# Kernel tuning notes

Hardware: AMD Instinct MI355X
Metric: run time of the kernel (lower is better)

The kernel has to match this reference:

```python
import jax, jax.numpy as jnp
import numpy as np

C_IMG = 16
GRID = 128
NV = 100000
NE = 1600000
CH = (32, 64, 64)
SCALE = 0.1
STEPS = 1
SLOPE = 0.3  # LeakyReLU default in module


def setup_inputs() -> dict:
    key = jax.random.key(0)
    ks = jax.random.split(key, 20)
    image_features = jax.random.normal(ks[0], (C_IMG, GRID, GRID, GRID), jnp.float32)
    # vertices live in voxel coordinates of the feature grid
    vertices = jax.random.uniform(ks[1], (NV, 3), jnp.float32) * (GRID - 1)
    edge_src = jax.random.randint(ks[2], (NE,), 0, NV, jnp.int32)
    edge_dst = jax.random.randint(ks[3], (NE,), 0, NV, jnp.int32)
    dims = [C_IMG + 3] + list(CH) + [3]  # +3 normalized positions
    inp = {"image_features": image_features, "vertices": vertices,
           "edge_src": edge_src, "edge_dst": edge_dst}
    ki = 4
    for i in range(len(dims) - 1):
        fan_in = dims[i]
        s = 1.0 / np.sqrt(fan_in)
        inp[f"w_self{i}"] = jax.random.normal(ks[ki], (dims[i], dims[i + 1]), jnp.float32) * s
        inp[f"w_nb{i}"] = jax.random.normal(ks[ki + 1], (dims[i], dims[i + 1]), jnp.float32) * s
        inp[f"b{i}"] = jnp.zeros((dims[i + 1],), jnp.float32)
        ki += 2
    return inp


def trilinear_sample(img, verts):
    # img: (C, W, H, D); verts: (V, 3) voxel coords -> (V, C)
    C, W, H, D = img.shape
    hi = jnp.array([W - 1, H - 1, D - 1], verts.dtype)
    p = jnp.clip(verts, 0.0, hi)
    p0 = jnp.floor(p)
    i0 = p0.astype(jnp.int32)
    i1 = jnp.minimum(i0 + 1, hi.astype(jnp.int32))
    w = p - p0
    x0, y0, z0 = i0[:, 0], i0[:, 1], i0[:, 2]
    x1, y1, z1 = i1[:, 0], i1[:, 1], i1[:, 2]
    wx, wy, wz = w[:, 0:1], w[:, 1:2], w[:, 2:3]

    def g(xi, yi, zi):
        return img[:, xi, yi, zi].T  # (V, C)

    c00 = g(x0, y0, z0) * (1 - wz) + g(x0, y0, z1) * wz
    c01 = g(x0, y1, z0) * (1 - wz) + g(x0, y1, z1) * wz
    c10 = g(x1, y0, z0) * (1 - wz) + g(x1, y0, z1) * wz
    c11 = g(x1, y1, z0) * (1 - wz) + g(x1, y1, z1) * wz
    return (c00 * (1 - wy) + c01 * wy) * (1 - wx) + (c10 * (1 - wy) + c11 * wy) * wx


def edge_conv(x, src, dst, inv_deg, w_self, w_nb, b):
    nb = jax.ops.segment_sum(x[src], dst, num_segments=x.shape[0]) * inv_deg
    return x @ w_self + nb @ w_nb + b


def reference(image_features, vertices, edge_src, edge_dst,
              w_self0, w_nb0, b0, w_self1, w_nb1, b1,
              w_self2, w_nb2, b2, w_self3, w_nb3, b3):
    nv = vertices.shape[0]
    deg = jax.ops.segment_sum(jnp.ones((edge_src.shape[0],), jnp.float32), edge_dst,
                              num_segments=nv)
    inv_deg = (1.0 / jnp.maximum(deg, 1.0))[:, None]
    grid_max = jnp.float32(max(image_features.shape[1:]))  # image_shape.max()
    layers = [(w_self0, w_nb0, b0), (w_self1, w_nb1, b1), (w_self2, w_nb2, b2)]
    for _ in range(STEPS):
        feats = trilinear_sample(image_features, vertices)
        feats = jnp.concatenate([vertices / grid_max, feats], axis=-1)
        h = feats
        for (ws, wn, b) in layers:
            h = jax.nn.leaky_relu(edge_conv(h, edge_src, edge_dst, inv_deg, ws, wn, b), SLOPE)
        deformation = edge_conv(h, edge_src, edge_dst, inv_deg, w_self3, w_nb3, b3)
        vertices = vertices + SCALE * deformation
    return vertices
```

## Files before the change

kernel.cpp:

```cpp
#include <hip/hip_runtime.h>

#define C_IMG 16
#define GRIDSZ 128
#define VOL (GRIDSZ * GRIDSZ * GRIDSZ)
#define SLOPE 0.3f
#define SCALE 0.1f
#define EPB 4096
#define CAPB 12288
#define BIN_CAP 16384

using f4_t  = __attribute__((ext_vector_type(4))) float;
using bf8_t = __attribute__((ext_vector_type(8))) short;

__device__ __forceinline__ unsigned int bf16_pack2(float a, float b) {
    unsigned int ua = __float_as_uint(a);
    ua = (ua + 0x7FFFu + ((ua >> 16) & 1u)) >> 16;
    unsigned int ub = __float_as_uint(b);
    ub = (ub + 0x7FFFu + ((ub >> 16) & 1u)) >> 16;
    return ua | (ub << 16);
}
__device__ __forceinline__ unsigned short bf16_1(float a) {
    unsigned int ua = __float_as_uint(a);
    return (unsigned short)((ua + 0x7FFFu + ((ua >> 16) & 1u)) >> 16);
}
__device__ __forceinline__ float bf_lo(unsigned int u) { return __uint_as_float(u << 16); }
__device__ __forceinline__ float bf_hi(unsigned int u) { return __uint_as_float(u & 0xFFFF0000u); }

__global__ __launch_bounds__(256) void k_transpose(const float* __restrict__ img,
                                                   unsigned int* __restrict__ timg) {
    const int t = blockIdx.x * 256 + threadIdx.x;
    const int zp = t & 63;
    const int xy = t >> 6;
    const size_t ibase = (size_t)xy * GRIDSZ + 2 * zp;
    float2 c[16];
    #pragma unroll
    for (int ch = 0; ch < 16; ++ch)
        c[ch] = *(const float2*)(img + (size_t)ch * VOL + ibase);
    uint4 o0a, o0b, o1a, o1b;
    o0a.x = bf16_pack2(c[0].x,  c[1].x);  o0a.y = bf16_pack2(c[2].x,  c[3].x);
    o0a.z = bf16_pack2(c[4].x,  c[5].x);  o0a.w = bf16_pack2(c[6].x,  c[7].x);
    o0b.x = bf16_pack2(c[8].x,  c[9].x);  o0b.y = bf16_pack2(c[10].x, c[11].x);
    o0b.z = bf16_pack2(c[12].x, c[13].x); o0b.w = bf16_pack2(c[14].x, c[15].x);
    o1a.x = bf16_pack2(c[0].y,  c[1].y);  o1a.y = bf16_pack2(c[2].y,  c[3].y);
    o1a.z = bf16_pack2(c[4].y,  c[5].y);  o1a.w = bf16_pack2(c[6].y,  c[7].y);
    o1b.x = bf16_pack2(c[8].y,  c[9].y);  o1b.y = bf16_pack2(c[10].y, c[11].y);
    o1b.z = bf16_pack2(c[12].y, c[13].y); o1b.w = bf16_pack2(c[14].y, c[15].y);
    unsigned int* po = timg + (size_t)(xy * GRIDSZ + 2 * zp) * 8;
    *(uint4*)(po + 0)  = o0a;
    *(uint4*)(po + 4)  = o0b;
    *(uint4*)(po + 8)  = o1a;
    *(uint4*)(po + 12) = o1b;
}

__global__ __launch_bounds__(256) void k_bucket(const int* __restrict__ esrc,
                                                const int* __restrict__ edst,
                                                int* __restrict__ bucketCursor,
                                                unsigned int* __restrict__ pairs,
                                                int* __restrict__ rowStart,
                                                int ne, int nv) {
    __shared__ unsigned int hist[256];
    __shared__ unsigned int pref[256];
    __shared__ unsigned int curs[256];
    __shared__ unsigned int gbase[256];
    __shared__ unsigned int stage_v[EPB];
    __shared__ unsigned char stage_b[EPB];
    const int tid = threadIdx.x;
    const int base = blockIdx.x * EPB;
    const int n = min(EPB, ne - base);
    if (blockIdx.x == 0 && tid == 0) rowStart[nv] = ne;
    hist[tid] = 0;
    __syncthreads();
    for (int i = tid; i < n; i += 256)
        atomicAdd(&hist[((unsigned)edst[base + i]) >> 9], 1u);
    __syncthreads();
    const unsigned int h = hist[tid];
    pref[tid] = h;
    __syncthreads();
    #pragma unroll
    for (int off = 1; off < 256; off <<= 1) {
        unsigned int t = (tid >= off) ? pref[tid - off] : 0;
        __syncthreads();
        pref[tid] += t;
        __syncthreads();
    }
    const unsigned int excl = pref[tid] - h;
    if (h) {
        int pos = atomicAdd(&bucketCursor[tid], (int)h);
        if (pos > CAPB - (int)h) pos = CAPB - (int)h;
        gbase[tid] = (unsigned int)(tid * CAPB + pos);
    } else {
        gbase[tid] = 0u;
    }
    __syncthreads();
    pref[tid] = excl;
    curs[tid] = excl;
    __syncthreads();
    for (int i = tid; i < n; i += 256) {
        unsigned int d = (unsigned)edst[base + i];
        unsigned int s = (unsigned)esrc[base + i];
        unsigned int p = atomicAdd(&curs[d >> 9], 1u);
        stage_v[p] = (s << 9) | (d & 511u);
        stage_b[p] = (unsigned char)(d >> 9);
    }
    __syncthreads();
    for (int i = tid; i < n; i += 256) {
        unsigned int b = stage_b[i];
        pairs[gbase[b] + (unsigned)i - pref[b]] = stage_v[i];
    }
}

__global__ __launch_bounds__(256) void k_binsort(const unsigned int* __restrict__ pairs,
                                                 const int* __restrict__ bucketCursor,
                                                 int* __restrict__ rowStart,
                                                 float* __restrict__ invdeg,
                                                 int* __restrict__ csrSrc, int nv) {
    __shared__ int deg_s[512];
    __shared__ int rs_s[512];
    __shared__ int cur_s[512];
    __shared__ int scan_s[256];
    __shared__ int bb[256];
    __shared__ int outbuf[BIN_CAP];
    const int tid = threadIdx.x;
    const int b = blockIdx.x;
    const int vbase = b << 9;
    if (vbase >= nv) return;
    const int nvb = min(512, nv - vbase);
    const int c = min(bucketCursor[tid], CAPB);
    bb[tid] = c;
    deg_s[tid] = 0;
    deg_s[tid + 256] = 0;
    __syncthreads();
    #pragma unroll
    for (int off = 1; off < 256; off <<= 1) {
        int t = (tid >= off) ? bb[tid - off] : 0;
        __syncthreads();
        bb[tid] += t;
        __syncthreads();
    }
    const int count = min(bucketCursor[b], CAPB);
    const int gs = bb[b] - count;
    const unsigned int* pbase = pairs + (size_t)b * CAPB;
    for (int i = tid; i < count; i += 256) {
        unsigned int p = pbase[i];
        atomicAdd(&deg_s[p & 511u], 1);
    }
    __syncthreads();
    const int d0 = deg_s[2 * tid];
    const int d1 = deg_s[2 * tid + 1];
    const int ps = d0 + d1;
    scan_s[tid] = ps;
    __syncthreads();
    #pragma unroll
    for (int off = 1; off < 256; off <<= 1) {
        int t = (tid >= off) ? scan_s[tid - off] : 0;
        __syncthreads();
        scan_s[tid] += t;
        __syncthreads();
    }
    const int epair = scan_s[tid] - ps;
    rs_s[2 * tid] = epair;
    rs_s[2 * tid + 1] = epair + d0;
    cur_s[2 * tid] = epair;
    cur_s[2 * tid + 1] = epair + d0;
    #pragma unroll
    for (int u = 0; u < 2; ++u) {
        int idx = 2 * tid + u;
        if (idx < nvb) {
            rowStart[vbase + idx] = gs + rs_s[idx];
            int d = deg_s[idx];
            invdeg[vbase + idx] = 1.0f / (float)(d > 1 ? d : 1);
        }
    }
    __syncthreads();
    for (int i = tid; i < count; i += 256) {
        unsigned int p = pbase[i];
        int pos = atomicAdd(&cur_s[p & 511u], 1);
        outbuf[pos] = (int)(p >> 9);
    }
    __syncthreads();
    for (int i = tid; i < count; i += 256) csrSrc[gs + i] = outbuf[i];
}

__global__ __launch_bounds__(256) void k_sample(const unsigned int* __restrict__ timg,
                                                const float* __restrict__ verts,
                                                unsigned int* __restrict__ feats, int nv) {
    int t = blockIdx.x * 256 + threadIdx.x;
    int v = t >> 1;
    int q = t & 1;
    if (v >= nv) return;
    float px = verts[v * 3 + 0];
    float py = verts[v * 3 + 1];
    float pz = verts[v * 3 + 2];
    float cx = fminf(fmaxf(px, 0.0f), 127.0f);
    float cy = fminf(fmaxf(py, 0.0f), 127.0f);
    float cz = fminf(fmaxf(pz, 0.0f), 127.0f);
    float fx = floorf(cx), fy = floorf(cy), fz = floorf(cz);
    int x0 = (int)fx, y0 = (int)fy, z0 = (int)fz;
    int x1 = min(x0 + 1, 127), y1 = min(y0 + 1, 127), z1 = min(z0 + 1, 127);
    float wx = cx - fx, wy = cy - fy, wz = cz - fz;
    const int qo = q * 4;
    #define LD(X, Y, Z) (*(const uint4*)(timg + ((size_t)((((X) << 7) + (Y)) << 7) + (size_t)(Z)) * 8 + qo))
    uint4 f000 = LD(x0, y0, z0), f001 = LD(x0, y0, z1);
    uint4 f010 = LD(x0, y1, z0), f011 = LD(x0, y1, z1);
    uint4 f100 = LD(x1, y0, z0), f101 = LD(x1, y0, z1);
    uint4 f110 = LD(x1, y1, z0), f111 = LD(x1, y1, z1);
    #undef LD
    float r[8];
    const unsigned int* a000 = (const unsigned int*)&f000;
    const unsigned int* a001 = (const unsigned int*)&f001;
    const unsigned int* a010 = (const unsigned int*)&f010;
    const unsigned int* a011 = (const unsigned int*)&f011;
    const unsigned int* a100 = (const unsigned int*)&f100;
    const unsigned int* a101 = (const unsigned int*)&f101;
    const unsigned int* a110 = (const unsigned int*)&f110;
    const unsigned int* a111 = (const unsigned int*)&f111;
    #pragma unroll
    for (int u = 0; u < 4; ++u) {
        float c00l = bf_lo(a000[u]) * (1.f - wz) + bf_lo(a001[u]) * wz;
        float c01l = bf_lo(a010[u]) * (1.f - wz) + bf_lo(a011[u]) * wz;
        float c10l = bf_lo(a100[u]) * (1.f - wz) + bf_lo(a101[u]) * wz;
        float c11l = bf_lo(a110[u]) * (1.f - wz) + bf_lo(a111[u]) * wz;
        r[2 * u] = (c00l * (1.f - wy) + c01l * wy) * (1.f - wx) +
                   (c10l * (1.f - wy) + c11l * wy) * wx;
        float c00h = bf_hi(a000[u]) * (1.f - wz) + bf_hi(a001[u]) * wz;
        float c01h = bf_hi(a010[u]) * (1.f - wz) + bf_hi(a011[u]) * wz;
        float c10h = bf_hi(a100[u]) * (1.f - wz) + bf_hi(a101[u]) * wz;
        float c11h = bf_hi(a110[u]) * (1.f - wz) + bf_hi(a111[u]) * wz;
        r[2 * u + 1] = (c00h * (1.f - wy) + c01h * wy) * (1.f - wx) +
                       (c10h * (1.f - wy) + c11h * wy) * wx;
    }
    unsigned int* row = feats + (size_t)v * 16;
    uint4 o;
    o.x = bf16_pack2(r[0], r[1]); o.y = bf16_pack2(r[2], r[3]);
    o.z = bf16_pack2(r[4], r[5]); o.w = bf16_pack2(r[6], r[7]);
    *(uint4*)(row + q * 4) = o;
    if (q == 0) {
        uint4 o2;
        o2.x = bf16_pack2(px * (1.0f / 128.0f), py * (1.0f / 128.0f));
        o2.y = bf16_pack2(pz * (1.0f / 128.0f), 0.0f);
        o2.z = 0u; o2.w = 0u;
        *(uint4*)(row + 8) = o2;
        *(uint4*)(row + 12) = make_uint4(0u, 0u, 0u, 0u);
    }
}

template <int KX, int COUT, bool REMAP0, int VALID_CIN, bool PREMUL>
__global__ __launch_bounds__(256) void k_layer_fused(const unsigned int* __restrict__ x,
                                                     const int* __restrict__ rowStart,
                                                     const int* __restrict__ csrSrc,
                                                     const float* __restrict__ invdeg,
                                                     const float* __restrict__ Ws,
                                                     const float* __restrict__ Wn,
                                                     const float* __restrict__ bias,
                                                     unsigned int* __restrict__ out, int nv,
                                                     const float* __restrict__ Wn3,
                                                     unsigned int* __restrict__ zout) {
    constexpr int KTOT = 2 * KX;
    constexpr int KW = KTOT + 8;
    constexpr int NT = COUT / 16;
    constexpr int MT = 2;
    constexpr int SXU = KX / 2;
    constexpr int KS = KX / 32;
    constexpr int VPB = 128;
    constexpr int NCH = KX / 8;
    constexpr int NBW = KX + 8;
    __shared__ __align__(16) unsigned short bt[COUT * KW];
    __shared__ __align__(16) unsigned short nb_s[VPB * NBW];
    __shared__ float wn3_s[192];

    for (int i = threadIdx.x; i < COUT * KTOT; i += 256) {
        int c = i / KTOT;
        int kk = i - c * KTOT;
        int j = (kk < KX) ? kk : kk - KX;
        const float* W = (kk < KX) ? Ws : Wn;
        float w = 0.f;
        if (j < VALID_CIN) {
            int sr = REMAP0 ? ((j < 16) ? (j + 3) : (j - 16)) : j;
            w = W[sr * COUT + c];
        }
        bt[c * KW + kk] = bf16_1(w);
    }
    if constexpr (PREMUL) {
        if (threadIdx.x < 192) wn3_s[threadIdx.x] = Wn3[threadIdx.x];
    }

    const int vb0 = blockIdx.x * VPB;
    for (int task = threadIdx.x; task < VPB * NCH; task += 256) {
        const int vloc = task / NCH;
        const int ch = task - vloc * NCH;
        const int v = vb0 + vloc;
        unsigned short* dst = nb_s + vloc * NBW + ch * 8;
        if (v < nv) {
            int beg = rowStart[v];
            int end = rowStart[v + 1];
            float a0 = 0.f, a1 = 0.f, a2 = 0.f, a3 = 0.f,
                  a4 = 0.f, a5 = 0.f, a6 = 0.f, a7 = 0.f;
            int j = beg;
            for (; j + 3 < end; j += 4) {
                int s0 = csrSrc[j];
                int s1 = csrSrc[j + 1];
                int s2 = csrSrc[j + 2];
                int s3 = csrSrc[j + 3];
                uint4 q0 = ((const uint4*)(x + (size_t)s0 * SXU))[ch];
                uint4 q1 = ((const uint4*)(x + (size_t)s1 * SXU))[ch];
                uint4 q2 = ((const uint4*)(x + (size_t)s2 * SXU))[ch];
                uint4 q3 = ((const uint4*)(x + (size_t)s3 * SXU))[ch];
                a0 += bf_lo(q0.x); a1 += bf_hi(q0.x);
                a2 += bf_lo(q0.y); a3 += bf_hi(q0.y);
                a4 += bf_lo(q0.z); a5 += bf_hi(q0.z);
                a6 += bf_lo(q0.w); a7 += bf_hi(q0.w);
                a0 += bf_lo(q1.x); a1 += bf_hi(q1.x);
                a2 += bf_lo(q1.y); a3 += bf_hi(q1.y);
                a4 += bf_lo(q1.z); a5 += bf_hi(q1.z);
                a6 += bf_lo(q1.w); a7 += bf_hi(q1.w);
                a0 += bf_lo(q2.x); a1 += bf_hi(q2.x);
                a2 += bf_lo(q2.y); a3 += bf_hi(q2.y);
                a4 += bf_lo(q2.z); a5 += bf_hi(q2.z);
                a6 += bf_lo(q2.w); a7 += bf_hi(q2.w);
                a0 += bf_lo(q3.x); a1 += bf_hi(q3.x);
                a2 += bf_lo(q3.y); a3 += bf_hi(q3.y);
                a4 += bf_lo(q3.z); a5 += bf_hi(q3.z);
                a6 += bf_lo(q3.w); a7 += bf_hi(q3.w);
            }
            for (; j < end; ++j) {
                int s = csrSrc[j];
                uint4 q = ((const uint4*)(x + (size_t)s * SXU))[ch];
                a0 += bf_lo(q.x); a1 += bf_hi(q.x);
                a2 += bf_lo(q.y); a3 += bf_hi(q.y);
                a4 += bf_lo(q.z); a5 += bf_hi(q.z);
                a6 += bf_lo(q.w); a7 += bf_hi(q.w);
            }
            const float id = invdeg[v];
            uint4 o;
            o.x = bf16_pack2(a0 * id, a1 * id); o.y = bf16_pack2(a2 * id, a3 * id);
            o.z = bf16_pack2(a4 * id, a5 * id); o.w = bf16_pack2(a6 * id, a7 * id);
            *(uint4*)dst = o;
        } else {
            *(uint4*)dst = make_uint4(0u, 0u, 0u, 0u);
        }
    }
    __syncthreads();

    const int lane = threadIdx.x & 63;
    const int wid = threadIdx.x >> 6;
    const int v0 = vb0 + wid * (MT * 16);
    const int row = lane & 15;
    const int kg = lane >> 4;

    f4_t acc[MT][NT] = {};

    #pragma unroll
    for (int ks = 0; ks < 2 * KS; ++ks) {
        bf8_t afrag[MT];
        if (ks < KS) {
            const int kbase = ks * 32;
            #pragma unroll
            for (int mt = 0; mt < MT; ++mt) {
                int v = v0 + mt * 16 + row;
                v = min(v, nv - 1);
                afrag[mt] = *(const bf8_t*)(x + (size_t)v * SXU + ((kbase + kg * 8) >> 1));
            }
        } else {
            const int kbase = (ks - KS) * 32;
            #pragma unroll
            for (int mt = 0; mt < MT; ++mt) {
                const int vloc = wid * (MT * 16) + mt * 16 + row;
                afrag[mt] = *(const bf8_t*)(nb_s + vloc * NBW + kbase + kg * 8);
            }
        }
        #pragma unroll
        for (int nt = 0; nt < NT; ++nt) {
            bf8_t bfrag = *(const bf8_t*)(bt + (nt * 16 + row) * KW + ks * 32 + kg * 8);
            #pragma unroll
            for (int mt = 0; mt < MT; ++mt)
                acc[mt][nt] = __builtin_amdgcn_mfma_f32_16x16x32_bf16(afrag[mt], bfrag,
                                                                      acc[mt][nt], 0, 0, 0);
        }
    }

    unsigned short* po = (unsigned short*)out;
    float bq[NT];
    #pragma unroll
    for (int nt = 0; nt < NT; ++nt) bq[nt] = bias[nt * 16 + row];
    #pragma unroll
    for (int mt = 0; mt < MT; ++mt) {
        #pragma unroll
        for (int r = 0; r < 4; ++r) {
            const int v = v0 + mt * 16 + kg * 4 + r;
            float tv[NT];
            #pragma unroll
            for (int nt = 0; nt < NT; ++nt) {
                float t = acc[mt][nt][r] + bq[nt];
                t = (t >= 0.f) ? t : SLOPE * t;
                tv[nt] = t;
                if (v < nv) po[(size_t)v * COUT + nt * 16 + row] = bf16_1(t);
            }
            if constexpr (PREMUL) {
                float z0 = 0.f, z1 = 0.f, z2 = 0.f;
                #pragma unroll
                for (int nt = 0; nt < NT; ++nt) {
                    const float* wr = wn3_s + (nt * 16 + row) * 3;
                    z0 += tv[nt] * wr[0];
                    z1 += tv[nt] * wr[1];
                    z2 += tv[nt] * wr[2];
                }
                #pragma unroll
                for (int m = 1; m < 16; m <<= 1) {
                    z0 += __shfl_xor(z0, m);
                    z1 += __shfl_xor(z1, m);
                    z2 += __shfl_xor(z2, m);
                }
                if (row == 0 && v < nv) {
                    uint2 o;
                    o.x = bf16_pack2(z0, z1);
                    o.y = bf16_pack2(z2, 0.f);
                    *(uint2*)(zout + (size_t)v * 2) = o;
                }
            }
        }
    }
}

__global__ __launch_bounds__(256) void k_final(const unsigned int* __restrict__ h,
                                               const unsigned int* __restrict__ z,
                                               const int* __restrict__ rowStart,
                                               const int* __restrict__ csrSrc,
                                               const float* __restrict__ invdeg,
                                               const float* __restrict__ ws,
                                               const float* __restrict__ b,
                                               const float* __restrict__ verts,
                                               float* __restrict__ out, int nv) {
    __shared__ float w_s[64 * 3];
    if (threadIdx.x < 64 * 3) w_s[threadIdx.x] = ws[threadIdx.x];
    __syncthreads();
    int v = blockIdx.x * 256 + threadIdx.x;
    if (v >= nv) return;
    float n0 = 0.f, n1 = 0.f, n2 = 0.f;
    {
        int beg = rowStart[v];
        int end = rowStart[v + 1];
        int j = beg;
        for (; j + 3 < end; j += 4) {
            int s0 = csrSrc[j];
            int s1 = csrSrc[j + 1];
            int s2 = csrSrc[j + 2];
            int s3 = csrSrc[j + 3];
            uint2 q0 = *(const uint2*)(z + (size_t)s0 * 2);
            uint2 q1 = *(const uint2*)(z + (size_t)s1 * 2);
            uint2 q2 = *(const uint2*)(z + (size_t)s2 * 2);
            uint2 q3 = *(const uint2*)(z + (size_t)s3 * 2);
            n0 += bf_lo(q0.x); n1 += bf_hi(q0.x); n2 += bf_lo(q0.y);
            n0 += bf_lo(q1.x); n1 += bf_hi(q1.x); n2 += bf_lo(q1.y);
            n0 += bf_lo(q2.x); n1 += bf_hi(q2.x); n2 += bf_lo(q2.y);
            n0 += bf_lo(q3.x); n1 += bf_hi(q3.x); n2 += bf_lo(q3.y);
        }
        for (; j < end; ++j) {
            int s = csrSrc[j];
            uint2 q = *(const uint2*)(z + (size_t)s * 2);
            n0 += bf_lo(q.x); n1 += bf_hi(q.x); n2 += bf_lo(q.y);
        }
    }
    const uint4* hr = (const uint4*)(h + (size_t)v * 32);
    float a0 = b[0], a1 = b[1], a2 = b[2];
    #pragma unroll
    for (int q = 0; q < 8; ++q) {
        uint4 hv = hr[q];
        float f[8] = {bf_lo(hv.x), bf_hi(hv.x), bf_lo(hv.y), bf_hi(hv.y),
                      bf_lo(hv.z), bf_hi(hv.z), bf_lo(hv.w), bf_hi(hv.w)};
        #pragma unroll
        for (int i = 0; i < 8; ++i) {
            int k = q * 8 + i;
            a0 += f[i] * w_s[k * 3 + 0];
            a1 += f[i] * w_s[k * 3 + 1];
            a2 += f[i] * w_s[k * 3 + 2];
        }
    }
    float id = invdeg[v];
    a0 += n0 * id; a1 += n1 * id; a2 += n2 * id;
    out[(size_t)v * 3 + 0] = verts[(size_t)v * 3 + 0] + SCALE * a0;
    out[(size_t)v * 3 + 1] = verts[(size_t)v * 3 + 1] + SCALE * a1;
    out[(size_t)v * 3 + 2] = verts[(size_t)v * 3 + 2] + SCALE * a2;
}

extern "C" void kernel_launch(void* const* d_in, const int* in_sizes, int n_in,
                              void* d_out, int out_size, void* d_ws, size_t ws_size,
                              hipStream_t stream) {
    const float* img   = (const float*)d_in[0];
    const float* verts = (const float*)d_in[1];
    const int*   esrc  = (const int*)d_in[2];
    const int*   edst  = (const int*)d_in[3];
    const float* ws0 = (const float*)d_in[4];
    const float* wn0 = (const float*)d_in[5];
    const float* b0  = (const float*)d_in[6];
    const float* ws1 = (const float*)d_in[7];
    const float* wn1 = (const float*)d_in[8];
    const float* b1  = (const float*)d_in[9];
    const float* ws2 = (const float*)d_in[10];
    const float* wn2 = (const float*)d_in[11];
    const float* b2  = (const float*)d_in[12];
    const float* ws3 = (const float*)d_in[13];
    const float* wn3 = (const float*)d_in[14];
    const float* b3  = (const float*)d_in[15];

    const int nv = in_sizes[1] / 3;
    const int ne = in_sizes[2];

    char* base = (char*)d_ws;
    size_t off = 0;
    auto alloc = [&](size_t bytes) -> void* {
        off = (off + 255) & ~(size_t)255;
        void* p = base + off;
        off += bytes;
        return p;
    };
    float* invdeg   = (float*)alloc((size_t)nv * 4);
    int*   rowStart = (int*)alloc((size_t)(nv + 1) * 4);
    int*   bucketCursor = (int*)alloc(256 * 4);
    int*   csrSrc   = (int*)alloc((size_t)ne * 4);
    unsigned int* pairs = (unsigned int*)alloc((size_t)256 * CAPB * 4);
    unsigned int* A   = (unsigned int*)alloc((size_t)nv * 32 * 4);
    unsigned int* B   = (unsigned int*)alloc((size_t)nv * 32 * 4);
    unsigned int* Z   = (unsigned int*)alloc((size_t)nv * 2 * 4);
    unsigned int* timg = (unsigned int*)alloc((size_t)VOL * 16 * 2);

    auto blocks = [](long long n) { return (int)((n + 255) / 256); };
    const int nbuckets = (nv + 511) >> 9;
    const int lb = (nv + 127) / 128;

    hipMemsetAsync(bucketCursor, 0, 256 * 4, stream);
    k_transpose<<<VOL / 2 / 256, 256, 0, stream>>>(img, timg);
    k_bucket<<<(ne + EPB - 1) / EPB, 256, 0, stream>>>(esrc, edst, bucketCursor,
                                                       pairs, rowStart, ne, nv);
    k_binsort<<<nbuckets, 256, 0, stream>>>(pairs, bucketCursor, rowStart, invdeg, csrSrc, nv);

    k_sample<<<blocks((long long)nv * 2), 256, 0, stream>>>(timg, verts, A, nv);

    k_layer_fused<32, 32, true, 19, false><<<lb, 256, 0, stream>>>(
        A, rowStart, csrSrc, invdeg, ws0, wn0, b0, B, nv, nullptr, nullptr);

    k_layer_fused<32, 64, false, 32, false><<<lb, 256, 0, stream>>>(
        B, rowStart, csrSrc, invdeg, ws1, wn1, b1, A, nv, nullptr, nullptr);

    k_layer_fused<64, 64, false, 64, true><<<lb, 256, 0, stream>>>(
        A, rowStart, csrSrc, invdeg, ws2, wn2, b2, B, nv, wn3, Z);

    k_final<<<blocks(nv), 256, 0, stream>>>(
        B, Z, rowStart, csrSrc, invdeg, ws3, b3, verts, (float*)d_out, nv);
}
```

Baseline: 437.8 us.

## Gather neighbor features from FP8 copies to halve edge-gather bandwidth

Each layer now also writes an FP8 (e4m3-style, software encoded) copy of its output features. The next layer's neighbor aggregation gathers 16 channels per 16-byte load from these copies instead of 8 bf16 channels. The aim is to cut the random-gather memory traffic over 1.6M edges. In exchange it adds software encode/decode ALU work and extra stores, and it lowers the precision of the aggregated features, which risks accuracy tolerance.

```diff
diff --git a/kernel.cpp b/kernel.cpp
--- a/kernel.cpp
+++ b/kernel.cpp
@@ -25,6 +25,32 @@
 }
 __device__ __forceinline__ float bf_lo(unsigned int u) { return __uint_as_float(u << 16); }
 __device__ __forceinline__ float bf_hi(unsigned int u) { return __uint_as_float(u & 0xFFFF0000u); }
+
+__device__ __forceinline__ float fp8_dec(unsigned int b) {
+    unsigned int em = b & 0x7Fu;
+    unsigned int bf = ((b & 0x80u) << 8) | ((em << 4) + 0x3C00u);
+    if (em < 8u) bf = (b & 0x80u) << 8;
+    return __uint_as_float(bf << 16);
+}
+__device__ __forceinline__ unsigned int fp8_enc(float f) {
+    unsigned int u = __float_as_uint(f);
+    unsigned int s = (u >> 24) & 0x80u;
+    int e = (int)((u >> 23) & 0xFFu) - 127 + 7;
+    unsigned int m = (u >> 20) & 0x7u;
+    unsigned int rem = u & 0xFFFFFu;
+    m += (rem > 0x80000u || (rem == 0x80000u && (m & 1u))) ? 1u : 0u;
+    if (m == 8u) { m = 0u; e += 1; }
+    if (e <= 0) return s;
+    if (e > 15) { e = 15; m = 6u; }
+    if (e == 15 && m == 7u) m = 6u;
+    return s | ((unsigned)e << 3) | m;
+}
+__device__ __forceinline__ void acc4(float* a, unsigned int w) {
+    a[0] += fp8_dec(w & 0xFFu);
+    a[1] += fp8_dec((w >> 8) & 0xFFu);
+    a[2] += fp8_dec((w >> 16) & 0xFFu);
+    a[3] += fp8_dec(w >> 24);
+}
 
 __global__ __launch_bounds__(256) void k_transpose(const float* __restrict__ img,
                                                    unsigned int* __restrict__ timg) {
@@ -183,7 +209,8 @@
 
 __global__ __launch_bounds__(256) void k_sample(const unsigned int* __restrict__ timg,
                                                 const float* __restrict__ verts,
-                                                unsigned int* __restrict__ feats, int nv) {
+                                                unsigned int* __restrict__ feats,
+                                                unsigned char* __restrict__ feats8, int nv) {
     int t = blockIdx.x * 256 + threadIdx.x;
     int v = t >> 1;
     int q = t & 1;
@@ -234,6 +261,11 @@
     o.x = bf16_pack2(r[0], r[1]); o.y = bf16_pack2(r[2], r[3]);
     o.z = bf16_pack2(r[4], r[5]); o.w = bf16_pack2(r[6], r[7]);
     *(uint4*)(row + q * 4) = o;
+    unsigned int w0 = fp8_enc(r[0]) | (fp8_enc(r[1]) << 8) |
+                      (fp8_enc(r[2]) << 16) | (fp8_enc(r[3]) << 24);
+    unsigned int w1 = fp8_enc(r[4]) | (fp8_enc(r[5]) << 8) |
+                      (fp8_enc(r[6]) << 16) | (fp8_enc(r[7]) << 24);
+    *(uint2*)(feats8 + (size_t)v * 32 + q * 8) = make_uint2(w0, w1);
     if (q == 0) {
         uint4 o2;
         o2.x = bf16_pack2(px * (1.0f / 128.0f), py * (1.0f / 128.0f));
@@ -241,18 +273,25 @@
         o2.z = 0u; o2.w = 0u;
         *(uint4*)(row + 8) = o2;
         *(uint4*)(row + 12) = make_uint4(0u, 0u, 0u, 0u);
-    }
-}
-
-template <int KX, int COUT, bool REMAP0, int VALID_CIN, bool PREMUL>
+        unsigned int wp = fp8_enc(px * (1.0f / 128.0f)) |
+                          (fp8_enc(py * (1.0f / 128.0f)) << 8) |
+                          (fp8_enc(pz * (1.0f / 128.0f)) << 16);
+        *(uint4*)(feats8 + (size_t)v * 32 + 16) = make_uint4(wp, 0u, 0u, 0u);
+    }
+}
+
+template <int KX, int COUT, bool REMAP0, int VALID_CIN, bool PREMUL, bool EMIT8>
 __global__ __launch_bounds__(256) void k_layer_fused(const unsigned int* __restrict__ x,
+                                                     const unsigned char* __restrict__ g8,
                                                      const int* __restrict__ rowStart,
                                                      const int* __restrict__ csrSrc,
                                                      const float* __restrict__ invdeg,
                                                      const float* __restrict__ Ws,
                                                      const float* __restrict__ Wn,
                                                      const float* __restrict__ bias,
-                                                     unsigned int* __restrict__ out, int nv,
+                                                     unsigned int* __restrict__ out,
+                                                     unsigned char* __restrict__ out8,
+                                                     int nv,
                                                      const float* __restrict__ Wn3,
                                                      unsigned int* __restrict__ zout) {
     constexpr int KTOT = 2 * KX;
@@ -262,7 +301,7 @@
     constexpr int SXU = KX / 2;
     constexpr int KS = KX / 32;
     constexpr int VPB = 128;
-    constexpr int NCH = KX / 8;
+    constexpr int NCH8 = KX / 16;
     constexpr int NBW = KX + 8;
     __shared__ __align__(16) unsigned short bt[COUT * KW];
     __shared__ __align__(16) unsigned short nb_s[VPB * NBW];
@@ -285,58 +324,48 @@
     }
 
     const int vb0 = blockIdx.x * VPB;
-    for (int task = threadIdx.x; task < VPB * NCH; task += 256) {
-        const int vloc = task / NCH;
-        const int ch = task - vloc * NCH;
+    for (int task = threadIdx.x; task < VPB * NCH8; task += 256) {
+        const int vloc = task / NCH8;
+        const int ch = task - vloc * NCH8;
         const int v = vb0 + vloc;
-        unsigned short* dst = nb_s + vloc * NBW + ch * 8;
+        unsigned short* dst = nb_s + vloc * NBW + ch * 16;
         if (v < nv) {
             int beg = rowStart[v];
             int end = rowStart[v + 1];
-            float a0 = 0.f, a1 = 0.f, a2 = 0.f, a3 = 0.f,
-                  a4 = 0.f, a5 = 0.f, a6 = 0.f, a7 = 0.f;
+            float a[16];
+            #pragma unroll
+            for (int i = 0; i < 16; ++i) a[i] = 0.f;
             int j = beg;
             for (; j + 3 < end; j += 4) {
                 int s0 = csrSrc[j];
                 int s1 = csrSrc[j + 1];
                 int s2 = csrSrc[j + 2];
                 int s3 = csrSrc[j + 3];
-                uint4 q0 = ((const uint4*)(x + (size_t)s0 * SXU))[ch];
-                uint4 q1 = ((const uint4*)(x + (size_t)s1 * SXU))[ch];
-                uint4 q2 = ((const uint4*)(x + (size_t)s2 * SXU))[ch];
-                uint4 q3 = ((const uint4*)(x + (size_t)s3 * SXU))[ch];
-                a0 += bf_lo(q0.x); a1 += bf_hi(q0.x);
-                a2 += bf_lo(q0.y); a3 += bf_hi(q0.y);
-                a4 += bf_lo(q0.z); a5 += bf_hi(q0.z);
-                a6 += bf_lo(q0.w); a7 += bf_hi(q0.w);
-                a0 += bf_lo(q1.x); a1 += bf_hi(q1.x);
-                a2 += bf_lo(q1.y); a3 += bf_hi(q1.y);
-                a4 += bf_lo(q1.z); a5 += bf_hi(q1.z);
-                a6 += bf_lo(q1.w); a7 += bf_hi(q1.w);
-                a0 += bf_lo(q2.x); a1 += bf_hi(q2.x);
-                a2 += bf_lo(q2.y); a3 += bf_hi(q2.y);
-                a4 += bf_lo(q2.z); a5 += bf_hi(q2.z);
-                a6 += bf_lo(q2.w); a7 += bf_hi(q2.w);
-                a0 += bf_lo(q3.x); a1 += bf_hi(q3.x);
-                a2 += bf_lo(q3.y); a3 += bf_hi(q3.y);
-                a4 += bf_lo(q3.z); a5 += bf_hi(q3.z);
-                a6 += bf_lo(q3.w); a7 += bf_hi(q3.w);
+                uint4 q0 = ((const uint4*)(g8 + (size_t)s0 * KX))[ch];
+                uint4 q1 = ((const uint4*)(g8 + (size_t)s1 * KX))[ch];
+                uint4 q2 = ((const uint4*)(g8 + (size_t)s2 * KX))[ch];
+                uint4 q3 = ((const uint4*)(g8 + (size_t)s3 * KX))[ch];
+                acc4(a + 0, q0.x); acc4(a + 4, q0.y); acc4(a + 8, q0.z); acc4(a + 12, q0.w);
+                acc4(a + 0, q1.x); acc4(a + 4, q1.y); acc4(a + 8, q1.z); acc4(a + 12, q1.w);
+                acc4(a + 0, q2.x); acc4(a + 4, q2.y); acc4(a + 8, q2.z); acc4(a + 12, q2.w);
+                acc4(a + 0, q3.x); acc4(a + 4, q3.y); acc4(a + 8, q3.z); acc4(a + 12, q3.w);
             }
             for (; j < end; ++j) {
                 int s = csrSrc[j];
-                uint4 q = ((const uint4*)(x + (size_t)s * SXU))[ch];
-                a0 += bf_lo(q.x); a1 += bf_hi(q.x);
-                a2 += bf_lo(q.y); a3 += bf_hi(q.y);
-                a4 += bf_lo(q.z); a5 += bf_hi(q.z);
-                a6 += bf_lo(q.w); a7 += bf_hi(q.w);
+                uint4 q = ((const uint4*)(g8 + (size_t)s * KX))[ch];
+                acc4(a + 0, q.x); acc4(a + 4, q.y); acc4(a + 8, q.z); acc4(a + 12, q.w);
             }
             const float id = invdeg[v];
-            uint4 o;
-            o.x = bf16_pack2(a0 * id, a1 * id); o.y = bf16_pack2(a2 * id, a3 * id);
-            o.z = bf16_pack2(a4 * id, a5 * id); o.w = bf16_pack2(a6 * id, a7 * id);
-            *(uint4*)dst = o;
+            uint4 o1, o2;
+            o1.x = bf16_pack2(a[0] * id, a[1] * id);  o1.y = bf16_pack2(a[2] * id, a[3] * id);
+            o1.z = bf16_pack2(a[4] * id, a[5] * id);  o1.w = bf16_pack2(a[6] * id, a[7] * id);
+            o2.x = bf16_pack2(a[8] * id, a[9] * id);  o2.y = bf16_pack2(a[10] * id, a[11] * id);
+            o2.z = bf16_pack2(a[12] * id, a[13] * id); o2.w = bf16_pack2(a[14] * id, a[15] * id);
+            *(uint4*)dst = o1;
+            *(uint4*)(dst + 8) = o2;
         } else {
             *(uint4*)dst = make_uint4(0u, 0u, 0u, 0u);
+            *(uint4*)(dst + 8) = make_uint4(0u, 0u, 0u, 0u);
         }
     }
     __syncthreads();
@@ -393,7 +422,11 @@
                 float t = acc[mt][nt][r] + bq[nt];
                 t = (t >= 0.f) ? t : SLOPE * t;
                 tv[nt] = t;
-                if (v < nv) po[(size_t)v * COUT + nt * 16 + row] = bf16_1(t);
+                if (v < nv) {
+                    po[(size_t)v * COUT + nt * 16 + row] = bf16_1(t);
+                    if constexpr (EMIT8)
+                        out8[(size_t)v * COUT + nt * 16 + row] = (unsigned char)fp8_enc(t);
+                }
             }
             if constexpr (PREMUL) {
                 float z0 = 0.f, z1 = 0.f, z2 = 0.f;
@@ -521,6 +554,9 @@
     unsigned int* A   = (unsigned int*)alloc((size_t)nv * 32 * 4);
     unsigned int* B   = (unsigned int*)alloc((size_t)nv * 32 * 4);
     unsigned int* Z   = (unsigned int*)alloc((size_t)nv * 2 * 4);
+    unsigned char* feats8 = (unsigned char*)alloc((size_t)nv * 32);
+    unsigned char* h1_8   = (unsigned char*)alloc((size_t)nv * 32);
+    unsigned char* h2_8   = (unsigned char*)alloc((size_t)nv * 64);
     unsigned int* timg = (unsigned int*)alloc((size_t)VOL * 16 * 2);
 
     auto blocks = [](long long n) { return (int)((n + 255) / 256); };
@@ -533,16 +569,16 @@
                                                        pairs, rowStart, ne, nv);
     k_binsort<<<nbuckets, 256, 0, stream>>>(pairs, bucketCursor, rowStart, invdeg, csrSrc, nv);
 
-    k_sample<<<blocks((long long)nv * 2), 256, 0, stream>>>(timg, verts, A, nv);
-
-    k_layer_fused<32, 32, true, 19, false><<<lb, 256, 0, stream>>>(
-        A, rowStart, csrSrc, invdeg, ws0, wn0, b0, B, nv, nullptr, nullptr);
-
-    k_layer_fused<32, 64, false, 32, false><<<lb, 256, 0, stream>>>(
-        B, rowStart, csrSrc, invdeg, ws1, wn1, b1, A, nv, nullptr, nullptr);
-
-    k_layer_fused<64, 64, false, 64, true><<<lb, 256, 0, stream>>>(
-        A, rowStart, csrSrc, invdeg, ws2, wn2, b2, B, nv, wn3, Z);
+    k_sample<<<blocks((long long)nv * 2), 256, 0, stream>>>(timg, verts, A, feats8, nv);
+
+    k_layer_fused<32, 32, true, 19, false, true><<<lb, 256, 0, stream>>>(
+        A, feats8, rowStart, csrSrc, invdeg, ws0, wn0, b0, B, h1_8, nv, nullptr, nullptr);
+
+    k_layer_fused<32, 64, false, 32, false, true><<<lb, 256, 0, stream>>>(
+        B, h1_8, rowStart, csrSrc, invdeg, ws1, wn1, b1, A, h2_8, nv, nullptr, nullptr);
+
+    k_layer_fused<64, 64, false, 64, true, false><<<lb, 256, 0, stream>>>(
+        A, h2_8, rowStart, csrSrc, invdeg, ws2, wn2, b2, B, nullptr, nv, wn3, Z);
 
     k_final<<<blocks(nv), 256, 0, stream>>>(
         B, Z, rowStart, csrSrc, invdeg, ws3, b3, verts, (float*)d_out, nv);
```

Result: slower. 497.4 us (+13.6%).
